# Performance work log

Measured on AMD Instinct MI355X. Metric: run time of the kernel, lower is better.

Reference implementation:

```python
import math
import jax, jax.numpy as jnp
import numpy as np

B, H, T, NH, D = 2, 4, 2048, 8192, 256
THETA = 65536.0  # rope_theta = 2**16
TWO_PI = 2.0 * math.pi


def get_freqs(n, theta):
    # quantize(arange(n), q=2) = floor(i/2)*2, so dim pairs share a frequency
    idx = jnp.arange(n, dtype=jnp.float32)
    q = jnp.floor(idx / 2.0) * 2.0
    return 1.0 / (theta ** (q / n)) / TWO_PI


def rope(phases, v):
    ph = (phases % 1.0) * TWO_PI
    c = jnp.cos(ph)
    s = jnp.sin(ph)
    # interleaved pair rotation: (-v1, v0, -v3, v2, ...)
    v_rot = jnp.stack((-v[..., 1::2], v[..., ::2]), axis=-1).reshape(v.shape)
    return v * c + v_rot * s


def setup_inputs() -> dict:
    key = jax.random.key(0)
    k1, k2, k3 = jax.random.split(key, 3)
    Q = jax.random.normal(k1, (B, H, T, NH), dtype=jnp.float32)
    K = jax.random.normal(k2, (B, H, T, NH), dtype=jnp.float32)
    V = jax.random.normal(k3, (B, 1, T, D), dtype=jnp.float32)
    return {"Q": Q, "K": K, "V": V}


def reference(Q, K, V):
    freqs = get_freqs(NH, THETA).reshape(1, 1, 1, NH)          # [1,1,1,NH]
    t = jnp.arange(T, dtype=jnp.float32).reshape(1, 1, T, 1)    # [1,1,T,1]
    phases = t * freqs                                          # [1,1,T,NH]
    Qr = rope(phases, Q)
    Kr = rope(phases, K)
    scores = jnp.einsum('bhtn,bhsn->bhts', Qr, Kr)              # [B,H,T,T]
    mask = jnp.tril(jnp.ones((T, T), dtype=bool), k=-1)         # strictly lower
    scores = jnp.where(mask, scores, jnp.float32(0.0))
    # V: [B,1,T,D] broadcasts over heads
    return jnp.matmul(scores, V)                                # [B,H,T,D]
```

## Files before the change

kernel.cpp:

```cpp
#include <hip/hip_runtime.h>
#include <hip/hip_bf16.h>

#define B_ 2
#define H_ 4
#define T_ 2048
#define NH_ 8192
#define D_ 256

typedef __attribute__((ext_vector_type(4))) float f32x4;
typedef __attribute__((ext_vector_type(8))) short bf16x8;
typedef __attribute__((ext_vector_type(4))) int i32x4;

__device__ __forceinline__ unsigned short f2bf(float f) {
    union { float f; unsigned u; } v;
    v.f = f;
    unsigned u = v.u;
    unsigned r = u + 0x7FFFu + ((u >> 16) & 1u);
    return (unsigned short)(r >> 16);
}

__global__ __launch_bounds__(256) void rope_cast_kernel(
    const float* __restrict__ Q, const float* __restrict__ K,
    unsigned short* __restrict__ Qb, unsigned short* __restrict__ Kb,
    int bh0)
{
    const long gid = (long)blockIdx.x * 256 + threadIdx.x;
    const int ng = NH_ / 8;
    const int n8 = (int)(gid % ng) * 8;
    const long row = gid / ng;
    const int t = (int)(row % T_);
    const int lbh = (int)(row / T_);

    const long in_off  = ((long)(bh0 + lbh) * T_ + t) * NH_ + n8;
    const long out_off = ((long)lbh * T_ + t) * NH_ + n8;

    float4 qa = *(const float4*)(Q + in_off);
    float4 qb4 = *(const float4*)(Q + in_off + 4);
    float4 ka = *(const float4*)(K + in_off);
    float4 kb4 = *(const float4*)(K + in_off + 4);
    float qv[8] = {qa.x, qa.y, qa.z, qa.w, qb4.x, qb4.y, qb4.z, qb4.w};
    float kv[8] = {ka.x, ka.y, ka.z, ka.w, kb4.x, kb4.y, kb4.z, kb4.w};

    union { i32x4 v; unsigned short u[8]; } qo, ko;
    const int p0 = n8 >> 1;
    const float tf = (float)t;
#pragma unroll
    for (int j = 0; j < 4; ++j) {
        float freq = exp2f(-(float)(p0 + j) * (1.0f / 256.0f)) * 0.15915494309189535f;
        float phase = tf * freq;
        float r = phase - floorf(phase);
        float ph = r * 6.283185307179586f;
        float c = __cosf(ph);
        float s = __sinf(ph);
        float qe = qv[2 * j], qodd = qv[2 * j + 1];
        float ke = kv[2 * j], kodd = kv[2 * j + 1];
        qo.u[2 * j]     = f2bf(qe * c - qodd * s);
        qo.u[2 * j + 1] = f2bf(qodd * c + qe * s);
        ko.u[2 * j]     = f2bf(ke * c - kodd * s);
        ko.u[2 * j + 1] = f2bf(kodd * c + ke * s);
    }
    *(i32x4*)(Qb + out_off) = qo.v;
    *(i32x4*)(Kb + out_off) = ko.v;
}

__global__ __launch_bounds__(256) void vcast_kernel(
    const float* __restrict__ V, unsigned short* __restrict__ Vt)
{
    __shared__ unsigned short tile[64][72];
    const int t0 = blockIdx.x * 64;
    const int d0 = blockIdx.y * 64;
    const int b = blockIdx.z;
    const int tid = threadIdx.x;
#pragma unroll
    for (int rr = 0; rr < 16; ++rr) {
        int tl = rr * 4 + (tid >> 6);
        int dl = tid & 63;
        float v = V[((long)b * T_ + (t0 + tl)) * D_ + d0 + dl];
        tile[dl][tl] = f2bf(v);
    }
    __syncthreads();
#pragma unroll
    for (int rr = 0; rr < 16; ++rr) {
        int dl = rr * 4 + (tid >> 6);
        int tl = tid & 63;
        Vt[((long)b * D_ + (d0 + dl)) * T_ + t0 + tl] = tile[dl][tl];
    }
}

#define GLD16(g, l) __builtin_amdgcn_global_load_lds(                         \
    (const __attribute__((address_space(1))) void*)(g),                       \
    (__attribute__((address_space(3))) void*)(l), 16, 0, 0)

#define STEP(RB, SB, t_, DO_STAGE, VMN) {                                     \
    bf16x8 af[8], bv[4];                                                      \
    _Pragma("unroll") for (int n = 0; n < 4; ++n)                             \
        bv[n] = *(const bf16x8*)&Bs[RB][wc * 64 + n * 16 + rofs][sl8];        \
    _Pragma("unroll") for (int m = 0; m < 8; ++m)                             \
        af[m] = *(const bf16x8*)&As[RB][wr * 128 + m * 16 + rofs][sl8];       \
    if (DO_STAGE) {                                                           \
        const long ko_ = (long)((t_) + 2) * 32;                               \
        GLD16(gA0 + ko_, &As[SB][0][0] + dst);                                \
        GLD16(gA1 + ko_, &As[SB][64][0] + dst);                               \
        GLD16(gA2 + ko_, &As[SB][128][0] + dst);                              \
        GLD16(gA3 + ko_, &As[SB][192][0] + dst);                              \
        GLD16(gB0 + ko_, &Bs[SB][0][0] + dst);                                \
        GLD16(gB1 + ko_, &Bs[SB][64][0] + dst);                               \
    }                                                                         \
    __builtin_amdgcn_s_setprio(1);                                            \
    _Pragma("unroll") for (int m = 0; m < 8; ++m)                             \
        _Pragma("unroll") for (int n = 0; n < 4; ++n)                         \
            acc[m][n] = __builtin_amdgcn_mfma_f32_16x16x32_bf16(              \
                af[m], bv[n], acc[m][n], 0, 0, 0);                            \
    __builtin_amdgcn_s_setprio(0);                                            \
    if ((VMN) == 6)      asm volatile("s_waitcnt vmcnt(6)" ::: "memory");     \
    else if ((VMN) == 0) asm volatile("s_waitcnt vmcnt(0)" ::: "memory");     \
    if ((VMN) >= 0) { __builtin_amdgcn_s_barrier();                           \
                      __builtin_amdgcn_sched_barrier(0); }                    \
}

__global__ __launch_bounds__(256, 2) void gemm1_kernel(
    const unsigned short* __restrict__ Qb, const unsigned short* __restrict__ Kb,
    unsigned short* __restrict__ S)
{
    __shared__ __align__(16) unsigned short As[3][256][32];
    __shared__ __align__(16) unsigned short Bs[3][128][32];

    const int nwg = gridDim.x;
    const int orig = blockIdx.x;
    const int wg = (orig & 7) * (nwg >> 3) + (orig >> 3);

    const int t72 = wg % 72;
    const int lbh = wg / 72;
    int it = (int)((sqrtf(4.0f * (float)t72 + 1.0f) - 1.0f) * 0.5f);
    while ((it + 1) * (it + 2) <= t72) ++it;
    while (it * (it + 1) > t72) --it;
    const int jt = t72 - it * (it + 1);

    const int tid = threadIdx.x;
    const int lane = tid & 63;
    const int wid = tid >> 6;
    const int wr = wid >> 1;
    const int wc = wid & 1;
    const int rofs = lane & 15;
    const int sl8 = (((lane >> 4) ^ ((lane >> 1) & 3))) << 3;

    const int ss8 = (((tid & 3) ^ ((tid >> 3) & 3))) << 3;
    const int dst = tid * 8;
    const unsigned short* Ab = Qb + (long)lbh * T_ * NH_ + (long)it * 256 * NH_;
    const unsigned short* Bb = Kb + (long)lbh * T_ * NH_ + (long)jt * 128 * NH_;
    const unsigned short* gA0 = Ab + (long)(tid >> 2) * NH_ + ss8;
    const unsigned short* gA1 = gA0 + 64L * NH_;
    const unsigned short* gA2 = gA0 + 128L * NH_;
    const unsigned short* gA3 = gA0 + 192L * NH_;
    const unsigned short* gB0 = Bb + (long)(tid >> 2) * NH_ + ss8;
    const unsigned short* gB1 = gB0 + 64L * NH_;

    f32x4 acc[8][4];
#pragma unroll
    for (int m = 0; m < 8; ++m)
#pragma unroll
        for (int n = 0; n < 4; ++n)
            acc[m][n] = (f32x4){0.f, 0.f, 0.f, 0.f};

    {
        GLD16(gA0, &As[0][0][0] + dst);
        GLD16(gA1, &As[0][64][0] + dst);
        GLD16(gA2, &As[0][128][0] + dst);
        GLD16(gA3, &As[0][192][0] + dst);
        GLD16(gB0, &Bs[0][0][0] + dst);
        GLD16(gB1, &Bs[0][64][0] + dst);
        GLD16(gA0 + 32, &As[1][0][0] + dst);
        GLD16(gA1 + 32, &As[1][64][0] + dst);
        GLD16(gA2 + 32, &As[1][128][0] + dst);
        GLD16(gA3 + 32, &As[1][192][0] + dst);
        GLD16(gB0 + 32, &Bs[1][0][0] + dst);
        GLD16(gB1 + 32, &Bs[1][64][0] + dst);
    }
    asm volatile("s_waitcnt vmcnt(6)" ::: "memory");
    __builtin_amdgcn_s_barrier();
    __builtin_amdgcn_sched_barrier(0);

#pragma unroll 1
    for (int t = 0; t < 252; t += 3) {
        STEP(0, 2, t,     true, 6)
        STEP(1, 0, t + 1, true, 6)
        STEP(2, 1, t + 2, true, 6)
    }
    STEP(0, 2, 252, true, 6)
    STEP(1, 0, 253, true, 6)
    STEP(2, 1, 254, false, 0)
    STEP(0, 0, 255, false, -1)

    unsigned short* Sp = S + (long)lbh * T_ * T_;
    const int r0 = it * 256 + wr * 128 + ((lane >> 4) << 2);
    const int c0 = jt * 128 + wc * 64 + (lane & 15);
#pragma unroll
    for (int m = 0; m < 8; ++m) {
#pragma unroll
        for (int i = 0; i < 4; ++i) {
            const int rr = r0 + m * 16 + i;
#pragma unroll
            for (int n = 0; n < 4; ++n) {
                const int cc = c0 + n * 16;
                float v = (cc < rr) ? acc[m][n][i] : 0.0f;
                Sp[(long)rr * T_ + cc] = f2bf(v);
            }
        }
    }
}

__device__ __forceinline__ void stage_tile(const unsigned short* g, long ldk,
                                           unsigned short* l, int tid)
{
    const int row = tid >> 2;
    const int col = (tid & 3) << 3;
    const unsigned short* g0 = g + (long)row * ldk + col;
    const unsigned short* g1 = g0 + 64 * ldk;
    unsigned short* l0 = l + tid * 8;
    unsigned short* l1 = l0 + 2048;
    GLD16(g0, l0);
    GLD16(g1, l1);
}

__global__ __launch_bounds__(256) void gemm2_kernel(
    const unsigned short* __restrict__ S, const unsigned short* __restrict__ Vt,
    float* __restrict__ Out, int bh0)
{
    const int jn = blockIdx.x;
    const int it = blockIdx.y;
    const int lbh = blockIdx.z;
    const int bh = bh0 + lbh;
    const int b = bh / H_;

    __shared__ __align__(16) unsigned short As2[2][128][32];
    __shared__ __align__(16) unsigned short Bs2[2][128][32];

    const unsigned short* A  = S + (long)lbh * T_ * T_ + (long)it * 128 * T_;
    const unsigned short* Bm = Vt + (long)b * D_ * T_ + (long)jn * 128 * T_;
    const int KT = (it + 1) * 4;

    const int tid = threadIdx.x;
    const int lane = tid & 63;
    const int wid = tid >> 6;
    const int wr = wid >> 1;
    const int wc = wid & 1;
    f32x4 acc[4][4];
#pragma unroll
    for (int m = 0; m < 4; ++m)
#pragma unroll
        for (int n = 0; n < 4; ++n)
            acc[m][n] = (f32x4){0.f, 0.f, 0.f, 0.f};
    const int rofs = lane & 15;
    const int kofs = (lane >> 4) * 8;
    stage_tile(A, T_, &As2[0][0][0], tid);
    stage_tile(Bm, T_, &Bs2[0][0][0], tid);
    int cur = 0;
    for (int kt = 0; kt < KT; ++kt) {
        __syncthreads();
        if (kt + 1 < KT) {
            stage_tile(A + (long)(kt + 1) * 32, T_, &As2[cur ^ 1][0][0], tid);
            stage_tile(Bm + (long)(kt + 1) * 32, T_, &Bs2[cur ^ 1][0][0], tid);
        }
        bf16x8 af[4], bfr[4];
#pragma unroll
        for (int m = 0; m < 4; ++m)
            af[m] = *(const bf16x8*)&As2[cur][wr * 64 + m * 16 + rofs][kofs];
#pragma unroll
        for (int n = 0; n < 4; ++n)
            bfr[n] = *(const bf16x8*)&Bs2[cur][wc * 64 + n * 16 + rofs][kofs];
#pragma unroll
        for (int m = 0; m < 4; ++m)
#pragma unroll
            for (int n = 0; n < 4; ++n)
                acc[m][n] = __builtin_amdgcn_mfma_f32_16x16x32_bf16(
                    af[m], bfr[n], acc[m][n], 0, 0, 0);
        cur ^= 1;
    }

    float* Op = Out + ((long)bh * T_ + it * 128) * D_ + jn * 128;
#pragma unroll
    for (int m = 0; m < 4; ++m) {
        const int rbase = wr * 64 + m * 16 + ((lane >> 4) << 2);
#pragma unroll
        for (int i = 0; i < 4; ++i) {
            const int rr = rbase + i;
#pragma unroll
            for (int n = 0; n < 4; ++n) {
                const int cc = wc * 64 + n * 16 + (lane & 15);
                Op[(long)rr * D_ + cc] = acc[m][n][i];
            }
        }
    }
}

extern "C" void kernel_launch(void* const* d_in, const int* in_sizes, int n_in,
                              void* d_out, int out_size, void* d_ws, size_t ws_size,
                              hipStream_t stream)
{
    const float* Q = (const float*)d_in[0];
    const float* K = (const float*)d_in[1];
    const float* V = (const float*)d_in[2];
    float* Out = (float*)d_out;

    const size_t vt_elems = (size_t)B_ * D_ * T_;
    auto need = [&](int c) {
        return 2 * vt_elems + (size_t)c * T_ * NH_ * 2 * 2
             + (size_t)c * T_ * T_ * 2;
    };
    int c;
    if      (ws_size >= need(8)) c = 8;
    else if (ws_size >= need(4)) c = 4;
    else if (ws_size >= need(2)) c = 2;
    else if (ws_size >= need(1)) c = 1;
    else return;

    unsigned short* Vt = (unsigned short*)d_ws;
    unsigned short* Qb = Vt + vt_elems;
    unsigned short* Kb = Qb + (size_t)c * T_ * NH_;
    unsigned short* Sb = Kb + (size_t)c * T_ * NH_;

    vcast_kernel<<<dim3(T_ / 64, D_ / 64, B_), 256, 0, stream>>>(V, Vt);

    for (int bh0 = 0; bh0 < B_ * H_; bh0 += c) {
        const long groups = (long)c * T_ * (NH_ / 8);
        rope_cast_kernel<<<(int)(groups / 256), 256, 0, stream>>>(Q, K, Qb, Kb, bh0);
        gemm1_kernel<<<dim3(c * 72), 256, 0, stream>>>(Qb, Kb, Sb);
        gemm2_kernel<<<dim3(2, 16, c), 256, 0, stream>>>(Sb, Vt, Out, bh0);
    }
}
```

Before: 792.9 us.

## Prefetch next k-step LDS fragments into double-buffered registers in gemm1

Result: faster. 776.0 us (-2.1%).

```diff
diff --git a/kernel.cpp b/kernel.cpp
--- a/kernel.cpp
+++ b/kernel.cpp
@@ -91,31 +91,38 @@
     (const __attribute__((address_space(1))) void*)(g),                       \
     (__attribute__((address_space(3))) void*)(l), 16, 0, 0)
 
-#define STEP(RB, SB, t_, DO_STAGE, VMN) {                                     \
-    bf16x8 af[8], bv[4];                                                      \
-    _Pragma("unroll") for (int n = 0; n < 4; ++n)                             \
-        bv[n] = *(const bf16x8*)&Bs[RB][wc * 64 + n * 16 + rofs][sl8];        \
-    _Pragma("unroll") for (int m = 0; m < 8; ++m)                             \
-        af[m] = *(const bf16x8*)&As[RB][wr * 128 + m * 16 + rofs][sl8];       \
-    if (DO_STAGE) {                                                           \
-        const long ko_ = (long)((t_) + 2) * 32;                               \
-        GLD16(gA0 + ko_, &As[SB][0][0] + dst);                                \
-        GLD16(gA1 + ko_, &As[SB][64][0] + dst);                               \
-        GLD16(gA2 + ko_, &As[SB][128][0] + dst);                              \
-        GLD16(gA3 + ko_, &As[SB][192][0] + dst);                              \
-        GLD16(gB0 + ko_, &Bs[SB][0][0] + dst);                                \
-        GLD16(gB1 + ko_, &Bs[SB][64][0] + dst);                               \
-    }                                                                         \
-    __builtin_amdgcn_s_setprio(1);                                            \
-    _Pragma("unroll") for (int m = 0; m < 8; ++m)                             \
-        _Pragma("unroll") for (int n = 0; n < 4; ++n)                         \
-            acc[m][n] = __builtin_amdgcn_mfma_f32_16x16x32_bf16(              \
-                af[m], bv[n], acc[m][n], 0, 0, 0);                            \
-    __builtin_amdgcn_s_setprio(0);                                            \
-    if ((VMN) == 6)      asm volatile("s_waitcnt vmcnt(6)" ::: "memory");     \
-    else if ((VMN) == 0) asm volatile("s_waitcnt vmcnt(0)" ::: "memory");     \
-    if ((VMN) >= 0) { __builtin_amdgcn_s_barrier();                           \
-                      __builtin_amdgcn_sched_barrier(0); }                    \
+#define PSTEP(CAF03, CAF47, CBV, NAF03, NBV, RB, NB, SB, t_, DO_STAGE, MODE) {  \
+    _Pragma("unroll") for (int m = 0; m < 4; ++m)                               \
+        CAF47[m] = *(const bf16x8*)&As[RB][wr * 128 + (m + 4) * 16 + rofs][sl8];\
+    if (DO_STAGE) {                                                             \
+        const long ko_ = (long)((t_) + 2) * 32;                                 \
+        GLD16(gA0 + ko_, &As[SB][0][0] + dst);                                  \
+        GLD16(gA1 + ko_, &As[SB][64][0] + dst);                                 \
+        GLD16(gA2 + ko_, &As[SB][128][0] + dst);                                \
+        GLD16(gA3 + ko_, &As[SB][192][0] + dst);                                \
+        GLD16(gB0 + ko_, &Bs[SB][0][0] + dst);                                  \
+        GLD16(gB1 + ko_, &Bs[SB][64][0] + dst);                                 \
+    }                                                                           \
+    __builtin_amdgcn_s_setprio(1);                                              \
+    _Pragma("unroll") for (int m = 0; m < 4; ++m)                               \
+        _Pragma("unroll") for (int n = 0; n < 4; ++n)                           \
+            acc[m][n] = __builtin_amdgcn_mfma_f32_16x16x32_bf16(                \
+                CAF03[m], CBV[n], acc[m][n], 0, 0, 0);                          \
+    _Pragma("unroll") for (int m = 0; m < 4; ++m)                               \
+        _Pragma("unroll") for (int n = 0; n < 4; ++n)                           \
+            acc[m + 4][n] = __builtin_amdgcn_mfma_f32_16x16x32_bf16(            \
+                CAF47[m], CBV[n], acc[m + 4][n], 0, 0, 0);                      \
+    __builtin_amdgcn_s_setprio(0);                                              \
+    if ((MODE) >= 0) {                                                          \
+        if ((MODE) == 6) asm volatile("s_waitcnt vmcnt(6)" ::: "memory");       \
+        else             asm volatile("s_waitcnt vmcnt(0)" ::: "memory");       \
+        __builtin_amdgcn_s_barrier();                                           \
+        __builtin_amdgcn_sched_barrier(0);                                      \
+        _Pragma("unroll") for (int m = 0; m < 4; ++m)                           \
+            NAF03[m] = *(const bf16x8*)&As[NB][wr * 128 + m * 16 + rofs][sl8];  \
+        _Pragma("unroll") for (int n = 0; n < 4; ++n)                           \
+            NBV[n] = *(const bf16x8*)&Bs[NB][wc * 64 + n * 16 + rofs][sl8];     \
+    }                                                                           \
 }
 
 __global__ __launch_bounds__(256, 2) void gemm1_kernel(
@@ -180,16 +187,28 @@
     __builtin_amdgcn_s_barrier();
     __builtin_amdgcn_sched_barrier(0);
 
+    bf16x8 af03x[4], af47x[4], bvx[4];
+    bf16x8 af03y[4], af47y[4], bvy[4];
+#pragma unroll
+    for (int m = 0; m < 4; ++m)
+        af03x[m] = *(const bf16x8*)&As[0][wr * 128 + m * 16 + rofs][sl8];
+#pragma unroll
+    for (int n = 0; n < 4; ++n)
+        bvx[n] = *(const bf16x8*)&Bs[0][wc * 64 + n * 16 + rofs][sl8];
+
 #pragma unroll 1
-    for (int t = 0; t < 252; t += 3) {
-        STEP(0, 2, t,     true, 6)
-        STEP(1, 0, t + 1, true, 6)
-        STEP(2, 1, t + 2, true, 6)
-    }
-    STEP(0, 2, 252, true, 6)
-    STEP(1, 0, 253, true, 6)
-    STEP(2, 1, 254, false, 0)
-    STEP(0, 0, 255, false, -1)
+    for (int t = 0; t < 252; t += 6) {
+        PSTEP(af03x, af47x, bvx, af03y, bvy, 0, 1, 2, t,     true, 6)
+        PSTEP(af03y, af47y, bvy, af03x, bvx, 1, 2, 0, t + 1, true, 6)
+        PSTEP(af03x, af47x, bvx, af03y, bvy, 2, 0, 1, t + 2, true, 6)
+        PSTEP(af03y, af47y, bvy, af03x, bvx, 0, 1, 2, t + 3, true, 6)
+        PSTEP(af03x, af47x, bvx, af03y, bvy, 1, 2, 0, t + 4, true, 6)
+        PSTEP(af03y, af47y, bvy, af03x, bvx, 2, 0, 1, t + 5, true, 6)
+    }
+    PSTEP(af03x, af47x, bvx, af03y, bvy, 0, 1, 2, 252, true, 6)
+    PSTEP(af03y, af47y, bvy, af03x, bvx, 1, 2, 0, 253, true, 6)
+    PSTEP(af03x, af47x, bvx, af03y, bvy, 2, 0, 1, 254, false, 0)
+    PSTEP(af03y, af47y, bvy, af03x, bvx, 0, 1, 2, 255, false, -1)
 
     unsigned short* Sp = S + (long)lbh * T_ * T_;
     const int r0 = it * 256 + wr * 128 + ((lane >> 4) << 2);
```
